# Kernel optimization log

Hardware: AMD Instinct MI355X
Metric: run time of the kernel (lower is better)

Reference implementation:

```python
import jax, jax.numpy as jnp
import numpy as np

B, CIN, CI, HH, WW = 32, 256, 128, 64, 64


def setup_inputs() -> dict:
    key = jax.random.key(0)
    ks = jax.random.split(key, 9)
    s_in = 1.0 / np.sqrt(CIN)
    s_mid = 1.0 / np.sqrt(CI)
    return {
        "x": jax.random.normal(ks[0], (B, CIN, HH, WW), jnp.float32),
        "Wv": jax.random.normal(ks[1], (CI, CIN), jnp.float32) * s_in,
        "bv": jnp.zeros((CI,), jnp.float32),
        "Wk": jax.random.normal(ks[2], (CI, CIN), jnp.float32) * s_in,
        "bk": jnp.zeros((CI,), jnp.float32),
        "Wq": jax.random.normal(ks[3], (CI, CIN), jnp.float32) * s_in,
        "bq": jnp.zeros((CI,), jnp.float32),
        "Wo": jax.random.normal(ks[4], (CIN, CI), jnp.float32) * s_mid,
        "bo": jnp.zeros((CIN,), jnp.float32),
    }


def _conv1x1(x, W, b):
    # x: [B, Cin, H, W], W: [Cout, Cin] -> [B, Cout, H, W]
    return jnp.einsum('bchw,oc->bohw', x, W) + b[None, :, None, None]


def reference(x, Wv, bv, Wk, bk, Wq, bq, Wo, bo):
    Bn, _, H, W = x.shape
    hw = H * W
    V = _conv1x1(x, Wv, bv).reshape(Bn, CI, hw)   # [B, Ci, HW]
    K = _conv1x1(x, Wk, bk).reshape(Bn, CI, hw)
    Q = _conv1x1(x, Wq, bq).reshape(Bn, CI, hw)
    G = jnp.einsum('bcn,bdn->bcd', V, K)          # [B, Ci, Ci] = V @ K^T
    scale = 1.0 / np.sqrt(CI * hw)
    A = jnp.einsum('bcd,bdn->bcn', jax.nn.sigmoid(G), Q) * scale  # [B, Ci, HW]
    A = A.reshape(Bn, CI, H, W)
    out = _conv1x1(A, Wo, bo) + x
    return out
```

## Files before the change

### kernel.cpp

```cpp
#include <hip/hip_runtime.h>


typedef unsigned int   u32;
typedef unsigned short u16;
typedef __bf16 bf16_t;
typedef bf16_t bf16x8 __attribute__((ext_vector_type(8)));
typedef u16    u16x8  __attribute__((ext_vector_type(8)));
typedef float  f32x4  __attribute__((ext_vector_type(4)));

#define SWZ(row, byte) ((byte) ^ (((row) & 7) << 4))
#define SWZ4(n, byte) ((byte) ^ ((((((n) >> 2) & 7) ^ (((n) & 3) << 1)) << 4)))
#define SCALE 1.3810679320049757e-3f
#define ZERO4 (f32x4){0.f, 0.f, 0.f, 0.f}

__device__ __forceinline__ u16 f2bf(float f) {
  u32 u = __builtin_bit_cast(u32, f);
  u32 r = (u + 0x7FFFu + ((u >> 16) & 1u)) >> 16;
  return (u16)r;
}
__device__ __forceinline__ float bf2f(u16 h) {
  u32 u = ((u32)h) << 16;
  return __builtin_bit_cast(float, u);
}
__device__ __forceinline__ uint2 pack4bf(float a, float b, float c, float d) {
  uint2 r;
  r.x = (u32)f2bf(a) | ((u32)f2bf(b) << 16);
  r.y = (u32)f2bf(c) | ((u32)f2bf(d) << 16);
  return r;
}
__device__ __forceinline__ f32x4 mfma16(bf16x8 a, bf16x8 b, f32x4 c) {
  return __builtin_amdgcn_mfma_f32_16x16x32_bf16(a, b, c, 0, 0, 0);
}
__device__ __forceinline__ bf16x8 ld_lds_frag(const char* base, int row, int rowbytes, int kbyte) {
  return *reinterpret_cast<const bf16x8*>(base + row * rowbytes + SWZ(row, kbyte));
}
__device__ __forceinline__ bf16x8 ld_lds_frag4(const char* base, int row, int rowbytes, int kbyte) {
  return *reinterpret_cast<const bf16x8*>(base + row * rowbytes + SWZ4(row, kbyte));
}
__device__ __forceinline__ bf16x8 ld_g_bf16frag(const u16* base, int row, int rowlen, int kelem) {
  return *reinterpret_cast<const bf16x8*>(base + (size_t)row * rowlen + kelem);
}
__device__ __forceinline__ bf16x8 ld_g_f32frag(const float* base, int row, int rowlen, int kelem) {
  const float* p = base + (size_t)row * rowlen + kelem;
  float4 v0 = *reinterpret_cast<const float4*>(p);
  float4 v1 = *reinterpret_cast<const float4*>(p + 4);
  u16x8 h;
  h[0] = f2bf(v0.x); h[1] = f2bf(v0.y); h[2] = f2bf(v0.z); h[3] = f2bf(v0.w);
  h[4] = f2bf(v1.x); h[5] = f2bf(v1.y); h[6] = f2bf(v1.z); h[7] = f2bf(v1.w);
  return __builtin_bit_cast(bf16x8, h);
}

__global__ __launch_bounds__(1024) void k1_xxt(const float* __restrict__ x,
                                               u16* __restrict__ P,
                                               float* __restrict__ s_p) {
  const int kc = blockIdx.x;
  const int b  = blockIdx.y;
  const float* Xb = x + (size_t)b * 1048576;
  __shared__ char sm[65536];
  const int t = threadIdx.x;
  const int lane = t & 63;
  const int w = t >> 6, wi = w >> 2, wj = w & 3;
  const int l15 = lane & 15, l4 = lane >> 4;
  const int sd = t >> 4;
  const int sn2 = (t & 15) * 8;
  const int nbase = kc * 512;

  f32x4 acc[4][4];
#pragma unroll
  for (int i = 0; i < 4; ++i)
#pragma unroll
    for (int j = 0; j < 4; ++j) acc[i][j] = ZERO4;
  float ssum[4] = {0.f, 0.f, 0.f, 0.f};
  float4 stg[4];

  auto issue = [&](int tt) {
    const int n0 = nbase + tt * 64;
#pragma unroll
    for (int i = 0; i < 4; ++i)
      stg[i] = *reinterpret_cast<const float4*>(Xb + (size_t)(sd + 64 * i) * 4096 + n0 + (t & 15) * 4);
  };
  auto commit = [&](int tt) {
    char* B = sm + (tt & 1) * 32768;
#pragma unroll
    for (int i = 0; i < 4; ++i) {
      const int d = sd + 64 * i;
      ssum[i] += stg[i].x + stg[i].y + stg[i].z + stg[i].w;
      *reinterpret_cast<uint2*>(B + d * 128 + SWZ(d, sn2)) = pack4bf(stg[i].x, stg[i].y, stg[i].z, stg[i].w);
    }
  };

  issue(0); commit(0);
  for (int tt = 0; tt < 8; ++tt) {
    if (tt < 7) issue(tt + 1);
    __syncthreads();
    const char* Bc = sm + (tt & 1) * 32768;
#pragma unroll
    for (int ks = 0; ks < 2; ++ks) {
      const int kbyte = ks * 64 + l4 * 16;
      bf16x8 fa[4], fb[4];
#pragma unroll
      for (int i = 0; i < 4; ++i) fa[i] = ld_lds_frag(Bc, (4 * wi + i) * 16 + l15, 128, kbyte);
#pragma unroll
      for (int j = 0; j < 4; ++j) fb[j] = ld_lds_frag(Bc, (4 * wj + j) * 16 + l15, 128, kbyte);
#pragma unroll
      for (int i = 0; i < 4; ++i)
#pragma unroll
        for (int j = 0; j < 4; ++j) acc[i][j] = mfma16(fa[i], fb[j], acc[i][j]);
    }
    if (tt < 7) commit(tt + 1);
  }

#pragma unroll
  for (int i = 0; i < 4; ++i) {
    float v = ssum[i];
    v += __shfl_xor(v, 1); v += __shfl_xor(v, 2);
    v += __shfl_xor(v, 4); v += __shfl_xor(v, 8);
    if (l15 == 0) s_p[(b * 8 + kc) * 256 + sd + 64 * i] = v;
  }
  u16* Pb = P + ((size_t)(b * 8 + kc)) * 65536;
#pragma unroll
  for (int i = 0; i < 4; ++i)
#pragma unroll
    for (int j = 0; j < 4; ++j) {
      const int r0 = 64 * wi + 16 * i + 4 * l4;
      const int c  = 64 * wj + 16 * j + l15;
      f32x4 v = acc[i][j];
      *reinterpret_cast<uint2*>(Pb + (size_t)c * 256 + r0) = pack4bf(v[0], v[1], v[2], v[3]);
    }
}

__global__ __launch_bounds__(256) void k2_sum(const u16* __restrict__ P, u16* __restrict__ C) {
  const size_t idx = ((size_t)blockIdx.x * 256 + threadIdx.x) * 8;
  const size_t b = idx >> 16, e = idx & 65535;
  const u16* base = P + b * 8 * 65536 + e;
  float acc[8];
#pragma unroll
  for (int q = 0; q < 8; ++q) acc[q] = 0.f;
#pragma unroll
  for (int kc = 0; kc < 8; ++kc) {
    uint4 v = *reinterpret_cast<const uint4*>(base + (size_t)kc * 65536);
    u32 a4[4] = {v.x, v.y, v.z, v.w};
#pragma unroll
    for (int q = 0; q < 4; ++q) {
      acc[2 * q]     += bf2f((u16)(a4[q] & 0xFFFFu));
      acc[2 * q + 1] += bf2f((u16)(a4[q] >> 16));
    }
  }
  uint4 o;
  o.x = (u32)f2bf(acc[0]) | ((u32)f2bf(acc[1]) << 16);
  o.y = (u32)f2bf(acc[2]) | ((u32)f2bf(acc[3]) << 16);
  o.z = (u32)f2bf(acc[4]) | ((u32)f2bf(acc[5]) << 16);
  o.w = (u32)f2bf(acc[6]) | ((u32)f2bf(acc[7]) << 16);
  *reinterpret_cast<uint4*>(C + b * 65536 + e) = o;
}

__global__ __launch_bounds__(512, 2) void k3_chain(
    const u16* __restrict__ C, const float* __restrict__ Wv, const float* __restrict__ bv,
    const float* __restrict__ Wk, const float* __restrict__ bk, const float* __restrict__ Wq,
    const float* __restrict__ bq, const float* __restrict__ Wo, const float* __restrict__ bo,
    const float* __restrict__ s_p, u16* __restrict__ Ng, float* __restrict__ dvec) {
  const int b = blockIdx.x >> 3, sl = blockIdx.x & 7;
  __shared__ char smA[65536 + 16384];
  __shared__ char smB[65536];
  __shared__ float s_l[256];
  __shared__ float wsv_s[128], wsk_s[128];
  const int t = threadIdx.x;
  const int lane = t & 63;
  const int w = t >> 6;
  const int l15 = lane & 15, l4 = lane >> 4;
  const u16* Cb = C + (size_t)b * 65536;

  if (t < 256) {
    float a = 0.f;
#pragma unroll
    for (int kc = 0; kc < 8; ++kc) a += s_p[(b * 8 + kc) * 256 + t];
    s_l[t] = a;
  }
  for (int it = 0; it < 16; ++it) {
    const int flat = it * 512 + t;
    const int row = flat >> 6, col4 = (flat & 63) * 4;
    float4 v = *reinterpret_cast<const float4*>(Wk + row * 256 + col4);
    *reinterpret_cast<uint2*>(smA + row * 512 + SWZ(row, col4 * 2)) = pack4bf(v.x, v.y, v.z, v.w);
  }
  __syncthreads();

  if (t < 256) {
    const float* W = (t < 128) ? Wv : Wk;
    const int r = t & 127;
    float a = 0.f;
#pragma unroll 4
    for (int q = 0; q < 256; q += 4) {
      float4 wv = *reinterpret_cast<const float4*>(W + r * 256 + q);
      a += wv.x * s_l[q] + wv.y * s_l[q + 1] + wv.z * s_l[q + 2] + wv.w * s_l[q + 3];
    }
    if (t < 128) wsv_s[r] = a; else wsk_s[r] = a;
  }

  {
    const int wi = w >> 1, wj = w & 1;
    f32x4 acc[4][4];
#pragma unroll
    for (int i = 0; i < 4; ++i)
#pragma unroll
      for (int j = 0; j < 4; ++j) acc[i][j] = ZERO4;
#pragma unroll
    for (int ks = 0; ks < 8; ++ks) {
      const int ke = ks * 32 + l4 * 8;
      bf16x8 fa[4], fb[4];
#pragma unroll
      for (int i = 0; i < 4; ++i) fa[i] = ld_g_bf16frag(Cb, 64 * wi + 16 * i + l15, 256, ke);
#pragma unroll
      for (int j = 0; j < 4; ++j) fb[j] = ld_lds_frag(smA, 64 * wj + 16 * j + l15, 512, ke * 2);
#pragma unroll
      for (int i = 0; i < 4; ++i)
#pragma unroll
        for (int j = 0; j < 4; ++j) acc[i][j] = mfma16(fa[i], fb[j], acc[i][j]);
    }
#pragma unroll
    for (int i = 0; i < 4; ++i)
#pragma unroll
      for (int j = 0; j < 4; ++j) {
        const int d  = 64 * wj + 16 * j + l15;
        const int p0 = 64 * wi + 16 * i + 4 * l4;
        f32x4 v = acc[i][j];
        *reinterpret_cast<uint2*>(smB + d * 512 + SWZ(d, p0 * 2)) = pack4bf(v[0], v[1], v[2], v[3]);
      }
  }
  __syncthreads();

  {
    const int wi = w >> 1, wj = w & 1;
    f32x4 acc[2][4];
#pragma unroll
    for (int i = 0; i < 2; ++i)
#pragma unroll
      for (int j = 0; j < 4; ++j) acc[i][j] = ZERO4;
#pragma unroll
    for (int ks = 0; ks < 8; ++ks) {
      const int ke = ks * 32 + l4 * 8;
      bf16x8 fa[2], fb[4];
#pragma unroll
      for (int i = 0; i < 2; ++i) fa[i] = ld_g_f32frag(Wv, 32 * wi + 16 * i + l15, 256, ke);
#pragma unroll
      for (int j = 0; j < 4; ++j) fb[j] = ld_lds_frag(smB, 64 * wj + 16 * j + l15, 512, ke * 2);
#pragma unroll
      for (int i = 0; i < 2; ++i)
#pragma unroll
        for (int j = 0; j < 4; ++j) acc[i][j] = mfma16(fa[i], fb[j], acc[i][j]);
    }
#pragma unroll
    for (int i = 0; i < 2; ++i)
#pragma unroll
      for (int j = 0; j < 4; ++j) {
        const int c0 = 32 * wi + 16 * i + 4 * l4;
        const int d  = 64 * wj + 16 * j + l15;
        const float bkd = bk[d];
        const float aux = wsk_s[d] + 4096.f * bkd;
        u16 h[4];
#pragma unroll
        for (int r = 0; r < 4; ++r) {
          const int c = c0 + r;
          float g = acc[i][j][r] + wsv_s[c] * bkd + bv[c] * aux;
          float sg;
          if (g >= 0.f) sg = 1.f / (1.f + expf(-g));
          else { float e = expf(g); sg = e / (1.f + e); }
          h[r] = f2bf(sg);
        }
        uint2 pk;
        pk.x = (u32)h[0] | ((u32)h[1] << 16);
        pk.y = (u32)h[2] | ((u32)h[3] << 16);
        *reinterpret_cast<uint2*>(smA + d * 256 + SWZ(d, c0 * 2)) = pk;
      }
  }
  __syncthreads();

  for (int it = 0; it < 16; ++it) {
    const int flat = it * 512 + t;
    const int row = flat >> 6, col4 = (flat & 63) * 4;
    float4 v = *reinterpret_cast<const float4*>(Wq + row * 256 + col4);
    float vv[4] = {v.x, v.y, v.z, v.w};
#pragma unroll
    for (int ii = 0; ii < 4; ++ii) {
      const int col = col4 + ii;
      *reinterpret_cast<u16*>(smB + col * 256 + SWZ(col, row * 2)) = f2bf(vv[ii]);
    }
  }

  {
    const int wr = w >> 2, wc = w & 3;
    f32x4 acc[2];
    acc[0] = ZERO4; acc[1] = ZERO4;
#pragma unroll
    for (int ks = 0; ks < 4; ++ks) {
      const int ke = ks * 32 + l4 * 8;
      bf16x8 fa = ld_g_f32frag(Wo, sl * 32 + 16 * wr + l15, 128, ke);
      bf16x8 fb[2];
#pragma unroll
      for (int jj = 0; jj < 2; ++jj) fb[jj] = ld_lds_frag(smA, 32 * wc + 16 * jj + l15, 256, ke * 2);
#pragma unroll
      for (int jj = 0; jj < 2; ++jj) acc[jj] = mfma16(fa, fb[jj], acc[jj]);
    }
#pragma unroll
    for (int jj = 0; jj < 2; ++jj) {
      const int o = 16 * wr + 4 * l4;
      const int d = 32 * wc + 16 * jj + l15;
#pragma unroll
      for (int r = 0; r < 4; ++r)
        *reinterpret_cast<u16*>(smA + 65536 + (o + r) * 256 + SWZ(o + r, d * 2)) = f2bf(acc[jj][r]);
    }
  }
  __syncthreads();

  if (t < 32) {
    float sum = 0.f;
#pragma unroll 4
    for (int d2 = 0; d2 < 128; ++d2)
      sum += bf2f(*reinterpret_cast<const u16*>(smA + 65536 + t * 256 + SWZ(t, d2 * 2))) * bq[d2];
    dvec[b * 256 + sl * 32 + t] = SCALE * sum + bo[sl * 32 + t];
  }

  {
    const int wr = w >> 2, wc = w & 3;
    f32x4 acc[4];
#pragma unroll
    for (int jj = 0; jj < 4; ++jj) acc[jj] = ZERO4;
#pragma unroll
    for (int ks = 0; ks < 4; ++ks) {
      const int kb = (ks * 32 + l4 * 8) * 2;
      bf16x8 fa = ld_lds_frag(smA + 65536, 16 * wr + l15, 256, kb);
      bf16x8 fb[4];
#pragma unroll
      for (int jj = 0; jj < 4; ++jj) fb[jj] = ld_lds_frag(smB, 64 * wc + 16 * jj + l15, 256, kb);
#pragma unroll
      for (int jj = 0; jj < 4; ++jj) acc[jj] = mfma16(fa, fb[jj], acc[jj]);
    }
    u16* Nb = Ng + (size_t)b * 65536;
#pragma unroll
    for (int jj = 0; jj < 4; ++jj) {
      const int o0 = sl * 32 + 16 * wr + 4 * l4;
      const int p  = 64 * wc + 16 * jj + l15;
#pragma unroll
      for (int r = 0; r < 4; ++r)
        Nb[(size_t)(o0 + r) * 256 + p] = f2bf(SCALE * acc[jj][r]);
    }
  }
}

__global__ __launch_bounds__(512) void k4_out(const float* __restrict__ x,
                                              const u16* __restrict__ Ng,
                                              const float* __restrict__ dvec,
                                              float* __restrict__ out) {
  const int b = blockIdx.x >> 5, nc = blockIdx.x & 31;
  __shared__ char Xt[32768];
  const int t = threadIdx.x, lane = t & 63, w = t >> 6;
  const int l15 = lane & 15, l4 = lane >> 4;
  const float* xb = x + (size_t)b * 1048576;
  float* ob = out + (size_t)b * 1048576;
  const u16* Nb = Ng + (size_t)b * 65536;

  bf16x8 bn[2][8];
  float dv[2];
#pragma unroll
  for (int j = 0; j < 2; ++j) {
    const int o = 32 * w + 16 * j + l15;
    dv[j] = dvec[b * 256 + o];
#pragma unroll
    for (int ks = 0; ks < 8; ++ks) bn[j][ks] = ld_g_bf16frag(Nb, o, 256, ks * 32 + l4 * 8);
  }

  float4 stg[4];
  auto issue = [&](int sub) {
    const int n0 = nc * 128 + sub * 32;
#pragma unroll
    for (int i = 0; i < 4; ++i) {
      const int p = (t >> 3) + 64 * i;
      stg[i] = *reinterpret_cast<const float4*>(xb + (size_t)p * 4096 + n0 + (t & 7) * 4);
    }
  };
  auto commit = [&](int sub) {
    char* B = Xt + (sub & 1) * 16384;
#pragma unroll
    for (int i = 0; i < 4; ++i) {
      const int p = (t >> 3) + 64 * i;
      float vv[4] = {stg[i].x, stg[i].y, stg[i].z, stg[i].w};
#pragma unroll
      for (int ii = 0; ii < 4; ++ii) {
        const int n = (t & 7) * 4 + ii;
        *reinterpret_cast<u16*>(B + n * 512 + SWZ4(n, p * 2)) = f2bf(vv[ii]);
      }
    }
  };

  issue(0); commit(0);
  for (int sub = 0; sub < 4; ++sub) {
    if (sub < 3) issue(sub + 1);
    __syncthreads();
    const char* Bc = Xt + (sub & 1) * 16384;
    const int n0 = nc * 128 + sub * 32;
    f32x4 acc[2][2];
#pragma unroll
    for (int i = 0; i < 2; ++i)
#pragma unroll
      for (int j = 0; j < 2; ++j) acc[i][j] = ZERO4;
#pragma unroll
    for (int ks = 0; ks < 8; ++ks) {
      bf16x8 fa[2];
#pragma unroll
      for (int i = 0; i < 2; ++i) fa[i] = ld_lds_frag4(Bc, 16 * i + l15, 512, (ks * 32 + l4 * 8) * 2);
#pragma unroll
      for (int i = 0; i < 2; ++i)
#pragma unroll
        for (int j = 0; j < 2; ++j) acc[i][j] = mfma16(fa[i], bn[j][ks], acc[i][j]);
    }
#pragma unroll
    for (int i = 0; i < 2; ++i)
#pragma unroll
      for (int j = 0; j < 2; ++j) {
        const int gn = n0 + 16 * i + 4 * l4;
        const int o  = 32 * w + 16 * j + l15;
        float4 res = *reinterpret_cast<const float4*>(xb + (size_t)o * 4096 + gn);
        float4 ov;
        ov.x = acc[i][j][0] + dv[j] + res.x;
        ov.y = acc[i][j][1] + dv[j] + res.y;
        ov.z = acc[i][j][2] + dv[j] + res.z;
        ov.w = acc[i][j][3] + dv[j] + res.w;
        *reinterpret_cast<float4*>(ob + (size_t)o * 4096 + gn) = ov;
      }
    if (sub < 3) commit(sub + 1);
  }
}

extern "C" void kernel_launch(void* const* d_in, const int* in_sizes, int n_in,
                              void* d_out, int out_size, void* d_ws, size_t ws_size,
                              hipStream_t stream) {
  (void)in_sizes; (void)n_in; (void)out_size; (void)ws_size;
  const float* x  = (const float*)d_in[0];
  const float* Wv = (const float*)d_in[1];
  const float* bv = (const float*)d_in[2];
  const float* Wk = (const float*)d_in[3];
  const float* bk = (const float*)d_in[4];
  const float* Wq = (const float*)d_in[5];
  const float* bq = (const float*)d_in[6];
  const float* Wo = (const float*)d_in[7];
  const float* bo = (const float*)d_in[8];
  float* out = (float*)d_out;

  char* ws = (char*)d_ws;
  u16*   P   = (u16*)(ws);
  u16*   C   = (u16*)(ws + 33554432);
  float* s_p = (float*)(ws + 37748736);
  u16*   Ng  = (u16*)(ws + 37781504);
  float* dv  = (float*)(ws + 41975808);

  hipLaunchKernelGGL(k1_xxt,  dim3(8, 32), dim3(1024), 0, stream, x, P, s_p);
  hipLaunchKernelGGL(k2_sum,  dim3(1024),  dim3(256),  0, stream, P, C);
  hipLaunchKernelGGL(k3_chain, dim3(256),  dim3(512),  0, stream,
                     C, Wv, bv, Wk, bk, Wq, bq, Wo, bo, s_p, Ng, dv);
  hipLaunchKernelGGL(k4_out,  dim3(1024),  dim3(512),  0, stream, x, Ng, dv, out);
}
```

Measured before the change: 152.8 us.

## Split k3 chain into 16 slices per batch with half-size LDS phases

The k3 chain kernel now runs 16 blocks per batch instead of 8, each producing 16 output rows. The Gram computation is reordered so that C·Wv^T is formed first in two 128-row phases and accumulated against Wk, with Wk and Wv read straight from global memory. This cuts LDS use so more blocks fit per CU. Wq^T staging is also split into two halves. In k4, the x staging is regrouped so each thread packs four channels into one 8-byte LDS store instead of sixteen 2-byte stores. The cost is redundant per-block Gram work across the 16 slices and more global weight reads.

```diff
diff --git a/kernel.cpp b/kernel.cpp
--- a/kernel.cpp
+++ b/kernel.cpp
@@ -154,14 +154,15 @@
   *reinterpret_cast<uint4*>(C + b * 65536 + e) = o;
 }
 
-__global__ __launch_bounds__(512, 2) void k3_chain(
+__global__ __launch_bounds__(512, 4) void k3_chain(
     const u16* __restrict__ C, const float* __restrict__ Wv, const float* __restrict__ bv,
     const float* __restrict__ Wk, const float* __restrict__ bk, const float* __restrict__ Wq,
     const float* __restrict__ bq, const float* __restrict__ Wo, const float* __restrict__ bo,
     const float* __restrict__ s_p, u16* __restrict__ Ng, float* __restrict__ dvec) {
-  const int b = blockIdx.x >> 3, sl = blockIdx.x & 7;
-  __shared__ char smA[65536 + 16384];
-  __shared__ char smB[65536];
+  const int b = blockIdx.x >> 4, sl = blockIdx.x & 15;
+  __shared__ char tbuf[32768];
+  __shared__ char gbuf[32768];
+  __shared__ char mbuf[4096];
   __shared__ float s_l[256];
   __shared__ float wsv_s[128], wsk_s[128];
   const int t = threadIdx.x;
@@ -175,12 +176,6 @@
 #pragma unroll
     for (int kc = 0; kc < 8; ++kc) a += s_p[(b * 8 + kc) * 256 + t];
     s_l[t] = a;
-  }
-  for (int it = 0; it < 16; ++it) {
-    const int flat = it * 512 + t;
-    const int row = flat >> 6, col4 = (flat & 63) * 4;
-    float4 v = *reinterpret_cast<const float4*>(Wk + row * 256 + col4);
-    *reinterpret_cast<uint2*>(smA + row * 512 + SWZ(row, col4 * 2)) = pack4bf(v.x, v.y, v.z, v.w);
   }
   __syncthreads();
 
@@ -196,154 +191,153 @@
     if (t < 128) wsv_s[r] = a; else wsk_s[r] = a;
   }
 
-  {
-    const int wi = w >> 1, wj = w & 1;
-    f32x4 acc[4][4];
-#pragma unroll
-    for (int i = 0; i < 4; ++i)
-#pragma unroll
-      for (int j = 0; j < 4; ++j) acc[i][j] = ZERO4;
+  const int wpA = w >> 2, wcA = w & 3;
+  const int wiB = w >> 1, wjB = w & 1;
+  auto phaseA = [&](int ph) {
+    f32x4 acc[4][2];
+#pragma unroll
+    for (int i = 0; i < 4; ++i) { acc[i][0] = ZERO4; acc[i][1] = ZERO4; }
 #pragma unroll
     for (int ks = 0; ks < 8; ++ks) {
       const int ke = ks * 32 + l4 * 8;
-      bf16x8 fa[4], fb[4];
-#pragma unroll
-      for (int i = 0; i < 4; ++i) fa[i] = ld_g_bf16frag(Cb, 64 * wi + 16 * i + l15, 256, ke);
-#pragma unroll
-      for (int j = 0; j < 4; ++j) fb[j] = ld_lds_frag(smA, 64 * wj + 16 * j + l15, 512, ke * 2);
+      bf16x8 fa[4], fb[2];
 #pragma unroll
       for (int i = 0; i < 4; ++i)
-#pragma unroll
-        for (int j = 0; j < 4; ++j) acc[i][j] = mfma16(fa[i], fb[j], acc[i][j]);
+        fa[i] = ld_g_bf16frag(Cb, 128 * ph + 64 * wpA + 16 * i + l15, 256, ke);
+#pragma unroll
+      for (int j = 0; j < 2; ++j)
+        fb[j] = ld_g_f32frag(Wv, 32 * wcA + 16 * j + l15, 256, ke);
+#pragma unroll
+      for (int i = 0; i < 4; ++i)
+#pragma unroll
+        for (int j = 0; j < 2; ++j) acc[i][j] = mfma16(fa[i], fb[j], acc[i][j]);
     }
 #pragma unroll
     for (int i = 0; i < 4; ++i)
 #pragma unroll
-      for (int j = 0; j < 4; ++j) {
-        const int d  = 64 * wj + 16 * j + l15;
-        const int p0 = 64 * wi + 16 * i + 4 * l4;
+      for (int j = 0; j < 2; ++j) {
+        const int pl0 = 64 * wpA + 16 * i + 4 * l4;
+        const int c   = 32 * wcA + 16 * j + l15;
         f32x4 v = acc[i][j];
-        *reinterpret_cast<uint2*>(smB + d * 512 + SWZ(d, p0 * 2)) = pack4bf(v[0], v[1], v[2], v[3]);
+        *reinterpret_cast<uint2*>(tbuf + c * 256 + SWZ(c, pl0 * 2)) = pack4bf(v[0], v[1], v[2], v[3]);
       }
-  }
-  __syncthreads();
-
-  {
-    const int wi = w >> 1, wj = w & 1;
-    f32x4 acc[2][4];
-#pragma unroll
-    for (int i = 0; i < 2; ++i)
-#pragma unroll
-      for (int j = 0; j < 4; ++j) acc[i][j] = ZERO4;
-#pragma unroll
-    for (int ks = 0; ks < 8; ++ks) {
+  };
+
+  f32x4 gacc[2][4];
+#pragma unroll
+  for (int i = 0; i < 2; ++i)
+#pragma unroll
+    for (int j = 0; j < 4; ++j) gacc[i][j] = ZERO4;
+  auto phaseB = [&](int ph) {
+#pragma unroll
+    for (int ks = 0; ks < 4; ++ks) {
       const int ke = ks * 32 + l4 * 8;
       bf16x8 fa[2], fb[4];
 #pragma unroll
-      for (int i = 0; i < 2; ++i) fa[i] = ld_g_f32frag(Wv, 32 * wi + 16 * i + l15, 256, ke);
-#pragma unroll
-      for (int j = 0; j < 4; ++j) fb[j] = ld_lds_frag(smB, 64 * wj + 16 * j + l15, 512, ke * 2);
-#pragma unroll
       for (int i = 0; i < 2; ++i)
-#pragma unroll
-        for (int j = 0; j < 4; ++j) acc[i][j] = mfma16(fa[i], fb[j], acc[i][j]);
-    }
-#pragma unroll
-    for (int i = 0; i < 2; ++i)
-#pragma unroll
-      for (int j = 0; j < 4; ++j) {
-        const int c0 = 32 * wi + 16 * i + 4 * l4;
-        const int d  = 64 * wj + 16 * j + l15;
-        const float bkd = bk[d];
-        const float aux = wsk_s[d] + 4096.f * bkd;
-        u16 h[4];
-#pragma unroll
-        for (int r = 0; r < 4; ++r) {
-          const int c = c0 + r;
-          float g = acc[i][j][r] + wsv_s[c] * bkd + bv[c] * aux;
-          float sg;
-          if (g >= 0.f) sg = 1.f / (1.f + expf(-g));
-          else { float e = expf(g); sg = e / (1.f + e); }
-          h[r] = f2bf(sg);
-        }
-        uint2 pk;
-        pk.x = (u32)h[0] | ((u32)h[1] << 16);
-        pk.y = (u32)h[2] | ((u32)h[3] << 16);
-        *reinterpret_cast<uint2*>(smA + d * 256 + SWZ(d, c0 * 2)) = pk;
+        fa[i] = ld_lds_frag(tbuf, 32 * wiB + 16 * i + l15, 256, ke * 2);
+#pragma unroll
+      for (int j = 0; j < 4; ++j)
+        fb[j] = ld_g_f32frag(Wk, 64 * wjB + 16 * j + l15, 256, 128 * ph + ke);
+#pragma unroll
+      for (int i = 0; i < 2; ++i)
+#pragma unroll
+        for (int j = 0; j < 4; ++j) gacc[i][j] = mfma16(fa[i], fb[j], gacc[i][j]);
+    }
+  };
+
+  phaseA(0);
+  __syncthreads();
+  phaseB(0);
+  __syncthreads();
+  phaseA(1);
+  __syncthreads();
+  phaseB(1);
+#pragma unroll
+  for (int i = 0; i < 2; ++i)
+#pragma unroll
+    for (int j = 0; j < 4; ++j) {
+      const int c0 = 32 * wiB + 16 * i + 4 * l4;
+      const int d  = 64 * wjB + 16 * j + l15;
+      const float bkd = bk[d];
+      const float aux = wsk_s[d] + 4096.f * bkd;
+      u16 h[4];
+#pragma unroll
+      for (int r = 0; r < 4; ++r) {
+        const int c = c0 + r;
+        float g = gacc[i][j][r] + wsv_s[c] * bkd + bv[c] * aux;
+        float sg;
+        if (g >= 0.f) sg = 1.f / (1.f + expf(-g));
+        else { float e = expf(g); sg = e / (1.f + e); }
+        h[r] = f2bf(sg);
       }
-  }
-  __syncthreads();
-
-  for (int it = 0; it < 16; ++it) {
-    const int flat = it * 512 + t;
-    const int row = flat >> 6, col4 = (flat & 63) * 4;
-    float4 v = *reinterpret_cast<const float4*>(Wq + row * 256 + col4);
-    float vv[4] = {v.x, v.y, v.z, v.w};
-#pragma unroll
-    for (int ii = 0; ii < 4; ++ii) {
-      const int col = col4 + ii;
-      *reinterpret_cast<u16*>(smB + col * 256 + SWZ(col, row * 2)) = f2bf(vv[ii]);
-    }
-  }
+      uint2 pk;
+      pk.x = (u32)h[0] | ((u32)h[1] << 16);
+      pk.y = (u32)h[2] | ((u32)h[3] << 16);
+      *reinterpret_cast<uint2*>(gbuf + d * 256 + SWZ(d, c0 * 2)) = pk;
+    }
+  __syncthreads();
 
   {
-    const int wr = w >> 2, wc = w & 3;
-    f32x4 acc[2];
-    acc[0] = ZERO4; acc[1] = ZERO4;
+    f32x4 acc = ZERO4;
 #pragma unroll
     for (int ks = 0; ks < 4; ++ks) {
       const int ke = ks * 32 + l4 * 8;
-      bf16x8 fa = ld_g_f32frag(Wo, sl * 32 + 16 * wr + l15, 128, ke);
-      bf16x8 fb[2];
-#pragma unroll
-      for (int jj = 0; jj < 2; ++jj) fb[jj] = ld_lds_frag(smA, 32 * wc + 16 * jj + l15, 256, ke * 2);
-#pragma unroll
-      for (int jj = 0; jj < 2; ++jj) acc[jj] = mfma16(fa, fb[jj], acc[jj]);
-    }
-#pragma unroll
-    for (int jj = 0; jj < 2; ++jj) {
-      const int o = 16 * wr + 4 * l4;
-      const int d = 32 * wc + 16 * jj + l15;
-#pragma unroll
-      for (int r = 0; r < 4; ++r)
-        *reinterpret_cast<u16*>(smA + 65536 + (o + r) * 256 + SWZ(o + r, d * 2)) = f2bf(acc[jj][r]);
-    }
-  }
-  __syncthreads();
-
-  if (t < 32) {
+      bf16x8 fa = ld_g_f32frag(Wo, sl * 16 + l15, 128, ke);
+      bf16x8 fb = ld_lds_frag(gbuf, 16 * w + l15, 256, ke * 2);
+      acc = mfma16(fa, fb, acc);
+    }
+    const int o = 4 * l4;
+    const int d = 16 * w + l15;
+#pragma unroll
+    for (int r = 0; r < 4; ++r)
+      *reinterpret_cast<u16*>(mbuf + (o + r) * 256 + SWZ(o + r, d * 2)) = f2bf(acc[r]);
+  }
+  auto stageWqT = [&](int ph) {
+#pragma unroll
+    for (int it = 0; it < 8; ++it) {
+      const int flat = it * 512 + t;
+      const int row = flat >> 5, pc = (flat & 31) * 4;
+      float4 v = *reinterpret_cast<const float4*>(Wq + row * 256 + 128 * ph + pc);
+      float vv[4] = {v.x, v.y, v.z, v.w};
+#pragma unroll
+      for (int ii = 0; ii < 4; ++ii) {
+        const int pl = pc + ii;
+        *reinterpret_cast<u16*>(tbuf + pl * 256 + SWZ(pl, row * 2)) = f2bf(vv[ii]);
+      }
+    }
+  };
+  stageWqT(0);
+  __syncthreads();
+
+  if (t < 16) {
     float sum = 0.f;
-#pragma unroll 4
     for (int d2 = 0; d2 < 128; ++d2)
-      sum += bf2f(*reinterpret_cast<const u16*>(smA + 65536 + t * 256 + SWZ(t, d2 * 2))) * bq[d2];
-    dvec[b * 256 + sl * 32 + t] = SCALE * sum + bo[sl * 32 + t];
-  }
-
-  {
-    const int wr = w >> 2, wc = w & 3;
-    f32x4 acc[4];
-#pragma unroll
-    for (int jj = 0; jj < 4; ++jj) acc[jj] = ZERO4;
+      sum += bf2f(*reinterpret_cast<const u16*>(mbuf + t * 256 + SWZ(t, d2 * 2))) * bq[d2];
+    dvec[b * 256 + sl * 16 + t] = SCALE * sum + bo[sl * 16 + t];
+  }
+
+  u16* Nb = Ng + (size_t)b * 65536;
+  auto phaseD = [&](int ph) {
+    f32x4 acc = ZERO4;
 #pragma unroll
     for (int ks = 0; ks < 4; ++ks) {
       const int kb = (ks * 32 + l4 * 8) * 2;
-      bf16x8 fa = ld_lds_frag(smA + 65536, 16 * wr + l15, 256, kb);
-      bf16x8 fb[4];
-#pragma unroll
-      for (int jj = 0; jj < 4; ++jj) fb[jj] = ld_lds_frag(smB, 64 * wc + 16 * jj + l15, 256, kb);
-#pragma unroll
-      for (int jj = 0; jj < 4; ++jj) acc[jj] = mfma16(fa, fb[jj], acc[jj]);
-    }
-    u16* Nb = Ng + (size_t)b * 65536;
-#pragma unroll
-    for (int jj = 0; jj < 4; ++jj) {
-      const int o0 = sl * 32 + 16 * wr + 4 * l4;
-      const int p  = 64 * wc + 16 * jj + l15;
-#pragma unroll
-      for (int r = 0; r < 4; ++r)
-        Nb[(size_t)(o0 + r) * 256 + p] = f2bf(SCALE * acc[jj][r]);
-    }
-  }
+      bf16x8 fa = ld_lds_frag(mbuf, l15, 256, kb);
+      bf16x8 fb = ld_lds_frag(tbuf, 16 * w + l15, 256, kb);
+      acc = mfma16(fa, fb, acc);
+    }
+    const int o0 = sl * 16 + 4 * l4;
+    const int p  = 128 * ph + 16 * w + l15;
+#pragma unroll
+    for (int r = 0; r < 4; ++r)
+      Nb[(size_t)(o0 + r) * 256 + p] = f2bf(SCALE * acc[r]);
+  };
+  phaseD(0);
+  __syncthreads();
+  stageWqT(1);
+  __syncthreads();
+  phaseD(1);
 }
 
 __global__ __launch_bounds__(512) void k4_out(const float* __restrict__ x,
@@ -368,27 +362,25 @@
     for (int ks = 0; ks < 8; ++ks) bn[j][ks] = ld_g_bf16frag(Nb, o, 256, ks * 32 + l4 * 8);
   }
 
+  const int p0 = (t >> 3) * 4;
+  const int nn = (t & 7) * 4;
   float4 stg[4];
   auto issue = [&](int sub) {
     const int n0 = nc * 128 + sub * 32;
 #pragma unroll
-    for (int i = 0; i < 4; ++i) {
-      const int p = (t >> 3) + 64 * i;
-      stg[i] = *reinterpret_cast<const float4*>(xb + (size_t)p * 4096 + n0 + (t & 7) * 4);
-    }
+    for (int q = 0; q < 4; ++q)
+      stg[q] = *reinterpret_cast<const float4*>(xb + (size_t)(p0 + q) * 4096 + n0 + nn);
   };
   auto commit = [&](int sub) {
     char* B = Xt + (sub & 1) * 16384;
-#pragma unroll
-    for (int i = 0; i < 4; ++i) {
-      const int p = (t >> 3) + 64 * i;
-      float vv[4] = {stg[i].x, stg[i].y, stg[i].z, stg[i].w};
-#pragma unroll
-      for (int ii = 0; ii < 4; ++ii) {
-        const int n = (t & 7) * 4 + ii;
-        *reinterpret_cast<u16*>(B + n * 512 + SWZ4(n, p * 2)) = f2bf(vv[ii]);
-      }
-    }
+    float vv0[4] = {stg[0].x, stg[1].x, stg[2].x, stg[3].x};
+    float vv1[4] = {stg[0].y, stg[1].y, stg[2].y, stg[3].y};
+    float vv2[4] = {stg[0].z, stg[1].z, stg[2].z, stg[3].z};
+    float vv3[4] = {stg[0].w, stg[1].w, stg[2].w, stg[3].w};
+    *reinterpret_cast<uint2*>(B + (nn + 0) * 512 + SWZ4(nn + 0, p0 * 2)) = pack4bf(vv0[0], vv0[1], vv0[2], vv0[3]);
+    *reinterpret_cast<uint2*>(B + (nn + 1) * 512 + SWZ4(nn + 1, p0 * 2)) = pack4bf(vv1[0], vv1[1], vv1[2], vv1[3]);
+    *reinterpret_cast<uint2*>(B + (nn + 2) * 512 + SWZ4(nn + 2, p0 * 2)) = pack4bf(vv2[0], vv2[1], vv2[2], vv2[3]);
+    *reinterpret_cast<uint2*>(B + (nn + 3) * 512 + SWZ4(nn + 3, p0 * 2)) = pack4bf(vv3[0], vv3[1], vv3[2], vv3[3]);
   };
 
   issue(0); commit(0);
@@ -454,7 +446,7 @@
 
   hipLaunchKernelGGL(k1_xxt,  dim3(8, 32), dim3(1024), 0, stream, x, P, s_p);
   hipLaunchKernelGGL(k2_sum,  dim3(1024),  dim3(256),  0, stream, P, C);
-  hipLaunchKernelGGL(k3_chain, dim3(256),  dim3(512),  0, stream,
+  hipLaunchKernelGGL(k3_chain, dim3(512),  dim3(512),  0, stream,
                      C, Wv, bv, Wk, bk, Wq, bq, Wo, bo, s_p, Ng, dv);
   hipLaunchKernelGGL(k4_out,  dim3(1024),  dim3(512),  0, stream, x, Ng, dv, out);
 }
```

Measured after the change: 320.9 us. 2.1x slower.
